# Optimization experiments

Hardware: AMD Instinct MI355X
Metric: run time of the kernel (lower is better)

The kernel has to match this reference:

```python
import jax, jax.numpy as jnp
import numpy as np

N_EMBED = 1024
HEAD_SIZE = 64
BLOCK_SIZE = 2048

def setup_inputs() -> dict:
    key = jax.random.key(0)
    kx, kq, kk, kv = jax.random.split(key, 4)
    scale = N_EMBED ** -0.5
    x = jax.random.normal(kx, (8, 2048, N_EMBED), dtype=jnp.float32)
    # nn.Linear weights stored as [out, in]; we keep [in, out] for x @ W
    Wq = jax.random.normal(kq, (N_EMBED, HEAD_SIZE), dtype=jnp.float32) * scale
    Wk = jax.random.normal(kk, (N_EMBED, HEAD_SIZE), dtype=jnp.float32) * scale
    Wv = jax.random.normal(kv, (N_EMBED, HEAD_SIZE), dtype=jnp.float32) * scale
    return {"x": x, "Wq": Wq, "Wk": Wk, "Wv": Wv}

def reference(x, Wq, Wk, Wv):
    B, T, C = x.shape
    q = x @ Wq  # [B,T,H]
    k = x @ Wk
    v = x @ Wv
    # NOTE: original scales by C**-0.5 (n_embed), not head_size**-0.5
    wei = jnp.einsum('bth,bsh->bts', q, k) * (C ** -0.5)  # [B,T,T]
    causal = jnp.tril(jnp.ones((T, T), dtype=bool))
    wei = jnp.where(causal, wei, -jnp.inf)
    wei = jax.nn.softmax(wei, axis=-1)
    out = jnp.einsum('bts,bsh->bth', wei, v)  # [B,T,H]
    return out
```

## Files before the change

kernel.cpp:

```cpp
#include <hip/hip_runtime.h>

#define B_ 8
#define T_ 2048
#define C_ 1024
#define H_ 64

typedef __attribute__((ext_vector_type(8))) short short8;
typedef __attribute__((ext_vector_type(4))) float floatx4;
typedef __attribute__((ext_vector_type(4))) int intx4;

static __device__ __forceinline__ unsigned short f2bf(float f) {
  unsigned int u = __builtin_bit_cast(unsigned int, f);
  u += 0x7FFFu + ((u >> 16) & 1u);
  return (unsigned short)(u >> 16);
}
static __device__ __forceinline__ unsigned short f2bf_t(float f) {
  return (unsigned short)(__builtin_bit_cast(unsigned int, f) >> 16);
}
static __device__ __forceinline__ float bf2f(unsigned short u) {
  return __builtin_bit_cast(float, ((unsigned int)u) << 16);
}
static __device__ __forceinline__ unsigned int fbits(float f) {
  return __builtin_bit_cast(unsigned int, f);
}

typedef const __attribute__((address_space(1))) unsigned int* gp1_t;
typedef __attribute__((address_space(3))) unsigned int* lp3_t;
static __device__ __forceinline__ void gl_lds16(const void* g, void* l) {
  __builtin_amdgcn_global_load_lds((gp1_t)g, (lp3_t)l, 16, 0, 0);
}

__global__ __launch_bounds__(256) void conv_w(const float* __restrict__ wq,
    const float* __restrict__ wk, const float* __restrict__ wv,
    unsigned short* __restrict__ wf) {
  int c = blockIdx.x * 256 + threadIdx.x;
  int lane = c & 63;
  int t = c >> 6;
  int ng = t % 12;
  int kk = t / 12;
  int k0 = kk * 32 + (lane >> 4) * 8;
  int n = ng * 16 + (lane & 15);
  const float* src;
  int col;
  float scale = 1.0f;
  if (n < 64)       { src = wq; col = n;       scale = 0.03125f * 1.44269504088896340736f; }
  else if (n < 128) { src = wk; col = n - 64;  }
  else              { src = wv; col = n - 128; }
  unsigned short o[8];
#pragma unroll
  for (int j = 0; j < 8; ++j) o[j] = f2bf(src[(size_t)(k0 + j) * H_ + col] * scale);
  *(uint4*)&wf[(size_t)c * 8] = *(const uint4*)o;
}

__global__ __launch_bounds__(256, 4) void qkv_proj(
    const float* __restrict__ x, const unsigned short* __restrict__ wf,
    unsigned short* __restrict__ qo, unsigned short* __restrict__ kf,
    unsigned short* __restrict__ vf) {
  __shared__ float XL[2][4096];
  int tid = threadIdx.x;
  int wave = tid >> 6, lane = tid & 63;
  int lane4 = lane & 15, quad = lane >> 4;
  int m0 = blockIdx.x * 32;
  int ph0 = blockIdx.x & 7;

  auto stage_ph = [&](int phr, int buf) {
#pragma unroll
    for (int j = 0; j < 4; ++j) {
      int c = (wave * 4 + j) * 64 + lane;
      int r = c >> 5, pc = c & 31;
      int cl = (pc & ~7) | ((pc ^ (r & 7)) & 7);
      gl_lds16(&x[(size_t)(m0 + r) * C_ + phr * 128 + cl * 4], &XL[buf][c * 4]);
    }
  };

  floatx4 acc[2][3];
#pragma unroll
  for (int mt = 0; mt < 2; ++mt)
#pragma unroll
    for (int nt = 0; nt < 3; ++nt) acc[mt][nt] = (floatx4)0.0f;

  stage_ph(ph0, 0);
  __syncthreads();

  for (int ph = 0; ph < 8; ++ph) {
    int buf = ph & 1;
    if (ph < 7) stage_ph((ph + 1 + ph0) & 7, buf ^ 1);
    int phr = (ph + ph0) & 7;
#pragma unroll
    for (int sl = 0; sl < 4; ++sl) {
      int s = phr * 4 + sl;
      short8 b[3];
#pragma unroll
      for (int nt = 0; nt < 3; ++nt)
        b[nt] = *(const short8*)&wf[(size_t)(s * 12 + wave * 3 + nt) * 512 + lane * 8];
      short8 a[2];
#pragma unroll
      for (int mt = 0; mt < 2; ++mt) {
        int r = mt * 16 + lane4;
        int c0 = sl * 8 + quad * 2;
        int pc0 = (c0 & ~7) | ((c0 ^ (r & 7)) & 7);
        int pc1 = ((c0 + 1) & ~7) | (((c0 + 1) ^ (r & 7)) & 7);
        float4 f0 = *(const float4*)&XL[buf][r * 128 + pc0 * 4];
        float4 f1 = *(const float4*)&XL[buf][r * 128 + pc1 * 4];
        intx4 pk;
        pk[0] = (int)__builtin_amdgcn_perm(fbits(f0.y), fbits(f0.x), 0x07060302u);
        pk[1] = (int)__builtin_amdgcn_perm(fbits(f0.w), fbits(f0.z), 0x07060302u);
        pk[2] = (int)__builtin_amdgcn_perm(fbits(f1.y), fbits(f1.x), 0x07060302u);
        pk[3] = (int)__builtin_amdgcn_perm(fbits(f1.w), fbits(f1.z), 0x07060302u);
        a[mt] = __builtin_bit_cast(short8, pk);
      }
#pragma unroll
      for (int mt = 0; mt < 2; ++mt)
#pragma unroll
        for (int nt = 0; nt < 3; ++nt)
          acc[mt][nt] = __builtin_amdgcn_mfma_f32_16x16x32_bf16(a[mt], b[nt], acc[mt][nt], 0, 0, 0);
    }
    __syncthreads();
  }

  unsigned short* VTB = (unsigned short*)&XL[0][0];
  unsigned short* KB  = VTB + 5120;
#pragma unroll
  for (int mt = 0; mt < 2; ++mt)
#pragma unroll
    for (int nt = 0; nt < 3; ++nt) {
      int n = wave * 48 + nt * 16 + lane4;
#pragma unroll
      for (int rr = 0; rr < 4; ++rr) {
        unsigned short val = f2bf(acc[mt][nt][rr]);
        int lrow = mt * 16 + quad * 4 + rr;
        if (n < 64)       qo[(size_t)(m0 + lrow) * H_ + n] = val;
        else if (n < 128) KB[lrow * 72 + (n - 64)] = val;
        else              VTB[(n - 128) * 40 + lrow] = val;
      }
    }
  __syncthreads();
  {
    int bb = m0 >> 11, t0 = m0 & 2047;
    int st = t0 >> 6, off = t0 & 63;
    int ks = tid >> 7, ctl = (tid >> 6) & 1, ln = tid & 63;
    int ct = (off >> 4) + ctl;
    int tl = ctl * 16 + (ln & 15);
    int h0 = ks * 32 + (ln >> 4) * 8;
    uint4 kd = *(const uint4*)&KB[tl * 72 + h0];
    *(uint4*)&kf[((size_t)((bb * 32 + st) * 2 + ks) * 4 + ct) * 512 + ln * 8] = kd;
    int nt = tid >> 6, l4 = tid & 15, qs = (tid >> 4) & 3;
    int ksv = off >> 5;
    uint4 vd = *(const uint4*)&VTB[(nt * 16 + l4) * 40 + qs * 8];
    *(uint4*)&vf[((size_t)((bb * 32 + st) * 2 + ksv) * 4 + nt) * 512 + (tid & 63) * 8] = vd;
  }
}

__global__ __launch_bounds__(512, 4) void attn(
    const unsigned short* __restrict__ qi, const unsigned short* __restrict__ Kf,
    const unsigned short* __restrict__ Vf, unsigned short* __restrict__ Op,
    float* __restrict__ lsum) {
  __shared__ unsigned short KV[2][8192];
  __shared__ unsigned short PL[8][16][72];

  int tid = threadIdx.x;
  int wave = tid >> 6, lane = tid & 63;
  int lane4 = lane & 15, quad = lane >> 4;
  int qt = 15 - (int)blockIdx.x;
  int b = blockIdx.y, split = blockIdx.z;
  int qb = qt * 128;
  int base = b * T_;

  int ntile = 2 * qt + 2;
  int sBeg = (split * ntile) >> 2;
  int sEnd = ((split + 1) * ntile) >> 2;

  short8 aq[2];
#pragma unroll
  for (int ks = 0; ks < 2; ++ks)
    aq[ks] = *(const short8*)&qi[(size_t)(base + qb + wave * 16 + lane4) * H_ + ks * 32 + quad * 8];

  float lrow[4];
  floatx4 o[4];
#pragma unroll
  for (int r = 0; r < 4; ++r) lrow[r] = 0.0f;
#pragma unroll
  for (int nt = 0; nt < 4; ++nt) o[nt] = (floatx4)0.0f;

  auto stage = [&](int st, int bf) {
    size_t tb = (size_t)(b * 32 + st) * 4096;
    gl_lds16(&Kf[tb + (size_t)tid * 8], &KV[bf][tid * 8]);
    gl_lds16(&Vf[tb + (size_t)tid * 8], &KV[bf][4096 + tid * 8]);
  };

  if (sBeg < sEnd) stage(sBeg, 0);
  __syncthreads();

  for (int st = sBeg; st < sEnd; ++st) {
    int buf = (st - sBeg) & 1;
    if (st + 1 < sEnd) stage(st + 1, buf ^ 1);

    floatx4 sacc[4];
#pragma unroll
    for (int ct = 0; ct < 4; ++ct) sacc[ct] = (floatx4)0.0f;
    __builtin_amdgcn_s_setprio(1);
#pragma unroll
    for (int ks = 0; ks < 2; ++ks)
#pragma unroll
      for (int ct = 0; ct < 4; ++ct) {
        short8 bk = *(const short8*)&KV[buf][(ks * 4 + ct) * 512 + lane * 8];
        sacc[ct] = __builtin_amdgcn_mfma_f32_16x16x32_bf16(aq[ks], bk, sacc[ct], 0, 0, 0);
      }
    __builtin_amdgcn_s_setprio(0);

    if (st >= 2 * qt) {
#pragma unroll
      for (int ct = 0; ct < 4; ++ct)
#pragma unroll
        for (int r = 0; r < 4; ++r) {
          int qrow = qb + wave * 16 + quad * 4 + r;
          int scol = st * 64 + ct * 16 + lane4;
          if (scol > qrow) sacc[ct][r] = -3.0e38f;
        }
    }

#pragma unroll
    for (int ct = 0; ct < 4; ++ct)
#pragma unroll
      for (int r = 0; r < 4; ++r) {
        float p = exp2f(sacc[ct][r] - 8.0f);
        lrow[r] += p;
        PL[wave][quad * 4 + r][ct * 16 + lane4] = f2bf_t(p);
      }

    __builtin_amdgcn_s_setprio(1);
#pragma unroll
    for (int ks = 0; ks < 2; ++ks) {
      short8 pa = *(const short8*)&PL[wave][lane4][ks * 32 + quad * 8];
#pragma unroll
      for (int nt = 0; nt < 4; ++nt) {
        short8 bv = *(const short8*)&KV[buf][4096 + (ks * 4 + nt) * 512 + lane * 8];
        o[nt] = __builtin_amdgcn_mfma_f32_16x16x32_bf16(pa, bv, o[nt], 0, 0, 0);
      }
    }
    __builtin_amdgcn_s_setprio(0);

    __syncthreads();
  }

#pragma unroll
  for (int off = 1; off < 16; off <<= 1)
#pragma unroll
    for (int r = 0; r < 4; ++r) lrow[r] += __shfl_xor(lrow[r], off);

  size_t pbase = (((size_t)split * 8 + b) * 16 + qt) * 128;
#pragma unroll
  for (int r = 0; r < 4; ++r) {
    int row = wave * 16 + quad * 4 + r;
#pragma unroll
    for (int nt = 0; nt < 4; ++nt)
      Op[(pbase + row) * 64 + nt * 16 + lane4] = f2bf(o[nt][r]);
    if (lane4 == 0) lsum[pbase + row] = lrow[r];
  }
}

__global__ __launch_bounds__(256) void merge_splits(
    const unsigned short* __restrict__ Op, const float* __restrict__ lsum,
    float* __restrict__ out) {
  int idx = blockIdx.x * 256 + threadIdx.x;
  int row = idx >> 4;
  int h4 = (idx & 15) * 4;
  int b = row >> 11, t = row & 2047;
  int qt = t >> 7, r = t & 127;
  float O0 = 0.f, O1 = 0.f, O2 = 0.f, O3 = 0.f, l = 0.f;
#pragma unroll
  for (int s = 0; s < 4; ++s) {
    size_t p = (((size_t)s * 8 + b) * 16 + qt) * 128 + r;
    l += lsum[p];
    ushort4 ov = *(const ushort4*)&Op[p * 64 + h4];
    O0 += bf2f(ov.x); O1 += bf2f(ov.y); O2 += bf2f(ov.z); O3 += bf2f(ov.w);
  }
  float inv = 1.0f / l;
  float4 res = make_float4(O0 * inv, O1 * inv, O2 * inv, O3 * inv);
  *(float4*)&out[(size_t)row * H_ + h4] = res;
}

extern "C" void kernel_launch(void* const* d_in, const int* in_sizes, int n_in,
                              void* d_out, int out_size, void* d_ws, size_t ws_size,
                              hipStream_t stream) {
  const float* x  = (const float*)d_in[0];
  const float* wq = (const float*)d_in[1];
  const float* wk = (const float*)d_in[2];
  const float* wv = (const float*)d_in[3];
  float* out = (float*)d_out;

  char* ws = (char*)d_ws;
  unsigned short* wf = (unsigned short*)ws;
  unsigned short* qb = (unsigned short*)(ws + 393216);
  unsigned short* kf = (unsigned short*)(ws + 2490368);
  unsigned short* vf = (unsigned short*)(ws + 4587520);
  unsigned short* Op = (unsigned short*)(ws + 6684672);
  float*          ls = (float*)(ws + 15073280);

  conv_w<<<96, 256, 0, stream>>>(wq, wk, wv, wf);
  qkv_proj<<<512, 256, 0, stream>>>(x, wf, qb, kf, vf);
  attn<<<dim3(16, 8, 4), 512, 0, stream>>>(qb, kf, vf, Op, ls);
  merge_splits<<<1024, 256, 0, stream>>>(Op, ls, out);
}
```

Baseline: 128.0 us.

## Compute transposed S tile so P feeds PV MFMA from registers

```diff
diff --git a/kernel.cpp b/kernel.cpp
--- a/kernel.cpp
+++ b/kernel.cpp
@@ -13,9 +13,6 @@
   unsigned int u = __builtin_bit_cast(unsigned int, f);
   u += 0x7FFFu + ((u >> 16) & 1u);
   return (unsigned short)(u >> 16);
-}
-static __device__ __forceinline__ unsigned short f2bf_t(float f) {
-  return (unsigned short)(__builtin_bit_cast(unsigned int, f) >> 16);
 }
 static __device__ __forceinline__ float bf2f(unsigned short u) {
   return __builtin_bit_cast(float, ((unsigned int)u) << 16);
@@ -146,7 +143,9 @@
     *(uint4*)&kf[((size_t)((bb * 32 + st) * 2 + ks) * 4 + ct) * 512 + ln * 8] = kd;
     int nt = tid >> 6, l4 = tid & 15, qs = (tid >> 4) & 3;
     int ksv = off >> 5;
-    uint4 vd = *(const uint4*)&VTB[(nt * 16 + l4) * 40 + qs * 8];
+    uint2 vlo = *(const uint2*)&VTB[(nt * 16 + l4) * 40 + qs * 4];
+    uint2 vhi = *(const uint2*)&VTB[(nt * 16 + l4) * 40 + 16 + qs * 4];
+    uint4 vd = make_uint4(vlo.x, vlo.y, vhi.x, vhi.y);
     *(uint4*)&vf[((size_t)((bb * 32 + st) * 2 + ksv) * 4 + nt) * 512 + (tid & 63) * 8] = vd;
   }
 }
@@ -156,7 +155,6 @@
     const unsigned short* __restrict__ Vf, unsigned short* __restrict__ Op,
     float* __restrict__ lsum) {
   __shared__ unsigned short KV[2][8192];
-  __shared__ unsigned short PL[8][16][72];
 
   int tid = threadIdx.x;
   int wave = tid >> 6, lane = tid & 63;
@@ -175,10 +173,8 @@
   for (int ks = 0; ks < 2; ++ks)
     aq[ks] = *(const short8*)&qi[(size_t)(base + qb + wave * 16 + lane4) * H_ + ks * 32 + quad * 8];
 
-  float lrow[4];
+  float lsumv = 0.0f;
   floatx4 o[4];
-#pragma unroll
-  for (int r = 0; r < 4; ++r) lrow[r] = 0.0f;
 #pragma unroll
   for (int nt = 0; nt < 4; ++nt) o[nt] = (floatx4)0.0f;
 
@@ -204,34 +200,42 @@
 #pragma unroll
       for (int ct = 0; ct < 4; ++ct) {
         short8 bk = *(const short8*)&KV[buf][(ks * 4 + ct) * 512 + lane * 8];
-        sacc[ct] = __builtin_amdgcn_mfma_f32_16x16x32_bf16(aq[ks], bk, sacc[ct], 0, 0, 0);
+        sacc[ct] = __builtin_amdgcn_mfma_f32_16x16x32_bf16(bk, aq[ks], sacc[ct], 0, 0, 0);
       }
     __builtin_amdgcn_s_setprio(0);
 
     if (st >= 2 * qt) {
+      int qrow = qb + wave * 16 + lane4;
 #pragma unroll
       for (int ct = 0; ct < 4; ++ct)
 #pragma unroll
         for (int r = 0; r < 4; ++r) {
-          int qrow = qb + wave * 16 + quad * 4 + r;
-          int scol = st * 64 + ct * 16 + lane4;
+          int scol = st * 64 + ct * 16 + quad * 4 + r;
           if (scol > qrow) sacc[ct][r] = -3.0e38f;
         }
     }
 
-#pragma unroll
-    for (int ct = 0; ct < 4; ++ct)
-#pragma unroll
-      for (int r = 0; r < 4; ++r) {
-        float p = exp2f(sacc[ct][r] - 8.0f);
-        lrow[r] += p;
-        PL[wave][quad * 4 + r][ct * 16 + lane4] = f2bf_t(p);
-      }
+    unsigned int pk[4][2];
+#pragma unroll
+    for (int ct = 0; ct < 4; ++ct) {
+      float p0 = exp2f(sacc[ct][0] - 8.0f);
+      float p1 = exp2f(sacc[ct][1] - 8.0f);
+      float p2 = exp2f(sacc[ct][2] - 8.0f);
+      float p3 = exp2f(sacc[ct][3] - 8.0f);
+      lsumv += (p0 + p1) + (p2 + p3);
+      pk[ct][0] = __builtin_amdgcn_perm(fbits(p1), fbits(p0), 0x07060302u);
+      pk[ct][1] = __builtin_amdgcn_perm(fbits(p3), fbits(p2), 0x07060302u);
+    }
 
     __builtin_amdgcn_s_setprio(1);
 #pragma unroll
     for (int ks = 0; ks < 2; ++ks) {
-      short8 pa = *(const short8*)&PL[wave][lane4][ks * 32 + quad * 8];
+      intx4 pai;
+      pai[0] = (int)pk[2 * ks][0];
+      pai[1] = (int)pk[2 * ks][1];
+      pai[2] = (int)pk[2 * ks + 1][0];
+      pai[3] = (int)pk[2 * ks + 1][1];
+      short8 pa = __builtin_bit_cast(short8, pai);
 #pragma unroll
       for (int nt = 0; nt < 4; ++nt) {
         short8 bv = *(const short8*)&KV[buf][4096 + (ks * 4 + nt) * 512 + lane * 8];
@@ -243,10 +247,8 @@
     __syncthreads();
   }
 
-#pragma unroll
-  for (int off = 1; off < 16; off <<= 1)
-#pragma unroll
-    for (int r = 0; r < 4; ++r) lrow[r] += __shfl_xor(lrow[r], off);
+  lsumv += __shfl_xor(lsumv, 16);
+  lsumv += __shfl_xor(lsumv, 32);
 
   size_t pbase = (((size_t)split * 8 + b) * 16 + qt) * 128;
 #pragma unroll
@@ -255,8 +257,8 @@
 #pragma unroll
     for (int nt = 0; nt < 4; ++nt)
       Op[(pbase + row) * 64 + nt * 16 + lane4] = f2bf(o[nt][r]);
-    if (lane4 == 0) lsum[pbase + row] = lrow[r];
-  }
+  }
+  if (quad == 0) lsum[pbase + wave * 16 + lane4] = lsumv;
 }
 
 __global__ __launch_bounds__(256) void merge_splits(
```

Result: no change. 125.5 us (-1.9%).
